# Kernel tuning notes

Hardware: AMD Instinct MI355X
Metric: run time of the kernel (lower is better)

Reference implementation:

```python
import jax, jax.numpy as jnp
import numpy as np

D_MODEL = 1024
NUM_HEADS = 16
D_K = D_MODEL // NUM_HEADS
SCALE = 1.0 / (D_K ** 0.5)


def setup_inputs() -> dict:
    key = jax.random.key(0)
    k1, k2, k3 = jax.random.split(key, 3)
    x = jax.random.normal(k1, (2, 2048, D_MODEL), dtype=jnp.float32)
    # torch nn.Linear weight layout: [out_features, in_features]; y = x @ W.T
    w_qkv = jax.random.normal(k2, (3 * D_MODEL, D_MODEL), dtype=jnp.float32) * (1.0 / np.sqrt(D_MODEL))
    w_out = jax.random.normal(k3, (D_MODEL, D_MODEL), dtype=jnp.float32) * (1.0 / np.sqrt(D_MODEL))
    return {"x": x, "w_qkv": w_qkv, "w_out": w_out}


def reference(x, w_qkv, w_out):
    b, s, _ = x.shape
    qkv = jnp.einsum("bsd,ed->bse", x, w_qkv)            # [b, s, 3*d_model]
    q, k, v = jnp.split(qkv, 3, axis=-1)
    # [b, s, h, d_k] -> [b, h, s, d_k]
    q = q.reshape(b, s, NUM_HEADS, D_K).transpose(0, 2, 1, 3)
    k = k.reshape(b, s, NUM_HEADS, D_K).transpose(0, 2, 1, 3)
    v = v.reshape(b, s, NUM_HEADS, D_K).transpose(0, 2, 1, 3)
    scores = jnp.einsum("bhqd,bhkd->bhqk", q, k) * SCALE   # [b, h, s, s]
    attn = jax.nn.softmax(scores, axis=-1)
    ctx = jnp.einsum("bhqk,bhkd->bhqd", attn, v)           # [b, h, s, d_k]
    ctx = ctx.transpose(0, 2, 1, 3).reshape(b, s, D_MODEL)
    return jnp.einsum("bsd,ed->bse", ctx, w_out)
```

## Files before the change

kernel.cpp:

```cpp
#include <hip/hip_runtime.h>

typedef __attribute__((ext_vector_type(8))) short bf16x8;
typedef __attribute__((ext_vector_type(4))) float f32x4;
typedef __attribute__((ext_vector_type(16))) float f32x16;
typedef __attribute__((ext_vector_type(4))) unsigned int u32x4;

#define MFMA16(A, B, C) __builtin_amdgcn_mfma_f32_16x16x32_bf16((A), (B), (C), 0, 0, 0)
#define MFMA32(A, B, C) __builtin_amdgcn_mfma_f32_32x32x16_bf16((A), (B), (C), 0, 0, 0)

static __device__ __forceinline__ unsigned short f32_to_bf16(float f) {
    unsigned int u = __builtin_bit_cast(unsigned int, f);
    u += 0x7fffu + ((u >> 16) & 1u);
    return (unsigned short)(u >> 16);
}

static __device__ __forceinline__ unsigned int cvtpk(float lo, float hi) {
    unsigned int r;
    asm("v_cvt_pk_bf16_f32 %0, %1, %2" : "=v"(r) : "v"(lo), "v"(hi));
    return r;
}

static __device__ __forceinline__ void gload16(const unsigned short* g, unsigned short* l) {
    __builtin_amdgcn_global_load_lds(
        (const __attribute__((address_space(1))) unsigned int*)g,
        (__attribute__((address_space(3))) unsigned int*)l, 16, 0, 0);
}

#define QSCALE 0.18033688011112042f

__global__ void cast3_f32_bf16(const float* __restrict__ x, const float* __restrict__ wq,
                               const float* __restrict__ wo,
                               unsigned short* __restrict__ xb, unsigned short* __restrict__ wqb,
                               unsigned short* __restrict__ wob) {
    int i = blockIdx.x * 256 + threadIdx.x;
    const float* src;
    unsigned short* dst;
    int off;
    if (i < 1048576)      { src = x;  dst = xb;  off = i; }
    else if (i < 1835008) { src = wq; dst = wqb; off = i - 1048576; }
    else                  { src = wo; dst = wob; off = i - 1835008; }
    float4 v = reinterpret_cast<const float4*>(src)[off];
    ushort4 o;
    o.x = f32_to_bf16(v.x);
    o.y = f32_to_bf16(v.y);
    o.z = f32_to_bf16(v.z);
    o.w = f32_to_bf16(v.w);
    reinterpret_cast<ushort4*>(dst)[off] = o;
}

template <int MODE>
__global__ __launch_bounds__(256, 2)
void gemm_bt(const unsigned short* __restrict__ Ag,
             const unsigned short* __restrict__ Bg,
             int N, int K,
             unsigned short* __restrict__ qO,
             unsigned short* __restrict__ kO,
             unsigned short* __restrict__ vO,
             float* __restrict__ fO)
{
    constexpr int BM = 128, BN = 128, BK = 64;
    __shared__ unsigned short sA[BM * BK];
    __shared__ unsigned short sB[BN * BK];

    const int m0 = blockIdx.y * BM;
    const int n0 = blockIdx.x * BN;
    const int t = threadIdx.x;
    const int lane = t & 63;
    const int wid = t >> 6;
    const int wr = wid >> 1, wc = wid & 1;
    const int g = lane >> 4, r = lane & 15;
    const int lr8 = lane >> 3, lc = lane & 7;

    const f32x4 fzero = {0.f, 0.f, 0.f, 0.f};
    f32x4 acc[4][4];
#pragma unroll
    for (int mi = 0; mi < 4; ++mi)
#pragma unroll
        for (int ni = 0; ni < 4; ++ni) acc[mi][ni] = fzero;

    for (int k0 = 0; k0 < K; k0 += BK) {
        __syncthreads();
#pragma unroll
        for (int rep = 0; rep < 4; ++rep) {
            const int rbase = rep * 32 + wid * 8;
            const int row = rbase + lr8;
            const int cs = lc ^ (row & 7);
            gload16(&Ag[(size_t)(m0 + row) * K + k0 + cs * 8], &sA[rbase * 64]);
            gload16(&Bg[(size_t)(n0 + row) * K + k0 + cs * 8], &sB[rbase * 64]);
        }
        __syncthreads();

#pragma unroll
        for (int ks = 0; ks < BK; ks += 32) {
            const int c = (ks >> 3) + g;
            bf16x8 af[4], bfr[4];
#pragma unroll
            for (int mi = 0; mi < 4; ++mi) {
                const int row = wr * 64 + mi * 16 + r;
                af[mi] = *reinterpret_cast<const bf16x8*>(&sA[row * BK + ((c * 8) ^ ((row & 7) * 8))]);
            }
#pragma unroll
            for (int ni = 0; ni < 4; ++ni) {
                const int row = wc * 64 + ni * 16 + r;
                bfr[ni] = *reinterpret_cast<const bf16x8*>(&sB[row * BK + ((c * 8) ^ ((row & 7) * 8))]);
            }
#pragma unroll
            for (int mi = 0; mi < 4; ++mi)
#pragma unroll
                for (int ni = 0; ni < 4; ++ni)
                    acc[mi][ni] = MFMA16(af[mi], bfr[ni], acc[mi][ni]);
        }
    }

#pragma unroll
    for (int mi = 0; mi < 4; ++mi) {
#pragma unroll
        for (int ni = 0; ni < 4; ++ni) {
            const int mbase = m0 + wr * 64 + mi * 16 + 4 * g;
            const int n = n0 + wc * 64 + ni * 16 + r;
            if (MODE == 0) {
                const int b = mbase >> 11, s = mbase & 2047;
                const int which = n >> 10;
                const int h = (n >> 6) & 15;
                const int d = n & 63;
                if (which == 2) {
                    ushort4 v4;
                    v4.x = f32_to_bf16(acc[mi][ni][0]);
                    v4.y = f32_to_bf16(acc[mi][ni][1]);
                    v4.z = f32_to_bf16(acc[mi][ni][2]);
                    v4.w = f32_to_bf16(acc[mi][ni][3]);
                    *reinterpret_cast<ushort4*>(&vO[(((size_t)(b * 16 + h)) * 64 + d) * 2048 + s]) = v4;
                } else {
                    const size_t dst = (((size_t)(b * 16 + h)) * 2048 + s) * 64 + d;
#pragma unroll
                    for (int i = 0; i < 4; ++i) {
                        const float val = acc[mi][ni][i];
                        if (which == 0) qO[dst + (size_t)i * 64] = f32_to_bf16(val * QSCALE);
                        else            kO[dst + (size_t)i * 64] = f32_to_bf16(val);
                    }
                }
            } else {
#pragma unroll
                for (int i = 0; i < 4; ++i)
                    fO[(size_t)(mbase + i) * N + n] = acc[mi][ni][i];
            }
        }
    }
}

__global__ __launch_bounds__(256, 2)
void attn_kernel(const unsigned short* __restrict__ Q,
                 const unsigned short* __restrict__ Kg,
                 const unsigned short* __restrict__ Vtg,
                 unsigned short* __restrict__ ctx)
{
    const int S = 2048;
    const int bid = blockIdx.x;
    const int swz = (bid & 7) * 64 + (bid >> 3);
    const int hb = swz >> 4;
    const int qb = swz & 15;
    const unsigned short* Qh = Q + (size_t)hb * S * 64;
    const unsigned short* Kh = Kg + (size_t)hb * S * 64;
    const unsigned short* Vh = Vtg + (size_t)hb * 64 * S;

    const int t = threadIdx.x, lane = t & 63, wid = t >> 6;
    const int l31 = lane & 31, lhi = lane >> 5;
    const int lr8 = lane >> 3, lc = lane & 7;
    const int q0 = qb * 128 + wid * 32;

    const int krow = (l31 & 19) | ((l31 & 4) << 1) | ((l31 & 8) >> 1);
    const int ksw = (krow & 7) ^ ((krow >> 3) & 3);
    const int vsw = (l31 & 7) ^ ((l31 >> 3) & 3);

    __shared__ unsigned short sK[2][64 * 64];
    __shared__ unsigned short sVt[2][64 * 64];

    bf16x8 qf[4];
#pragma unroll
    for (int dstep = 0; dstep < 4; ++dstep)
        qf[dstep] = *reinterpret_cast<const bf16x8*>(
            &Qh[(size_t)(q0 + l31) * 64 + dstep * 16 + lhi * 8]);

    f32x16 acc[2];
#pragma unroll
    for (int dt = 0; dt < 2; ++dt)
#pragma unroll
        for (int i = 0; i < 16; ++i) acc[dt][i] = 0.f;
    float mrun = -1e30f, lrun = 0.f;

#define STAGE(buf, k0)                                                                   \
    {                                                                                    \
        _Pragma("unroll")                                                                \
        for (int rep = 0; rep < 2; ++rep) {                                              \
            const int rbase = wid * 16 + rep * 8;                                        \
            const int row = rbase + lr8;                                                 \
            const int cs = lc ^ ((row & 7) ^ ((row >> 3) & 3));                          \
            gload16(&Kh[(size_t)((k0) + row) * 64 + cs * 8], &sK[buf][rbase * 64]);      \
            gload16(&Vh[(size_t)row * S + (k0) + cs * 8], &sVt[buf][rbase * 64]);        \
        }                                                                                \
    }

    STAGE(0, 0);
    int cur = 0;

    for (int it = 0; it < 32; ++it) {
        __syncthreads();
        if (it < 31) {
            const int kn = (it + 1) * 64;
            if (cur) STAGE(0, kn) else STAGE(1, kn);
        }

        f32x16 st0, st1;
#pragma unroll
        for (int i = 0; i < 16; ++i) { st0[i] = 0.f; st1[i] = 0.f; }
        __builtin_amdgcn_s_setprio(1);
#pragma unroll
        for (int dstep = 0; dstep < 4; ++dstep) {
            const int c = dstep * 2 + lhi;
            bf16x8 kf0 = *reinterpret_cast<const bf16x8*>(
                &sK[cur][krow * 64 + ((c ^ ksw) * 8)]);
            bf16x8 kf1 = *reinterpret_cast<const bf16x8*>(
                &sK[cur][(32 + krow) * 64 + ((c ^ ksw) * 8)]);
            st0 = MFMA32(kf0, qf[dstep], st0);
            st1 = MFMA32(kf1, qf[dstep], st1);
        }
        __builtin_amdgcn_s_setprio(0);

        float m8[8];
#pragma unroll
        for (int j = 0; j < 8; ++j)
            m8[j] = fmaxf(fmaxf(st0[j], st0[j + 8]), fmaxf(st1[j], st1[j + 8]));
        float m4a = fmaxf(m8[0], m8[1]), m4b = fmaxf(m8[2], m8[3]);
        float m4c = fmaxf(m8[4], m8[5]), m4d = fmaxf(m8[6], m8[7]);
        float mx = fmaxf(fmaxf(m4a, m4b), fmaxf(m4c, m4d));
        mx = fmaxf(mx, __shfl_xor(mx, 32));

        if (!__all(mx - mrun <= 8.f)) {
            const float mnew = fmaxf(mrun, mx);
            const float alpha = __builtin_amdgcn_exp2f(mrun - mnew);
            mrun = mnew;
            lrun *= alpha;
#pragma unroll
            for (int dt = 0; dt < 2; ++dt)
#pragma unroll
                for (int i = 0; i < 16; ++i) acc[dt][i] *= alpha;
        }

#pragma unroll
        for (int i = 0; i < 16; ++i) {
            st0[i] = __builtin_amdgcn_exp2f(st0[i] - mrun);
            st1[i] = __builtin_amdgcn_exp2f(st1[i] - mrun);
        }
        float s8[8];
#pragma unroll
        for (int j = 0; j < 8; ++j)
            s8[j] = (st0[j] + st0[j + 8]) + (st1[j] + st1[j + 8]);
        float sum = ((s8[0] + s8[1]) + (s8[2] + s8[3])) + ((s8[4] + s8[5]) + (s8[6] + s8[7]));
        sum += __shfl_xor(sum, 32);
        lrun += sum;

        bf16x8 pf[4];
#define PACK8(stv, base, out)                                                  \
        {                                                                      \
            u32x4 wv;                                                          \
            wv[0] = cvtpk(stv[(base) + 0], stv[(base) + 1]);                   \
            wv[1] = cvtpk(stv[(base) + 2], stv[(base) + 3]);                   \
            wv[2] = cvtpk(stv[(base) + 4], stv[(base) + 5]);                   \
            wv[3] = cvtpk(stv[(base) + 6], stv[(base) + 7]);                   \
            out = __builtin_bit_cast(bf16x8, wv);                              \
        }
        PACK8(st0, 0, pf[0])
        PACK8(st0, 8, pf[1])
        PACK8(st1, 0, pf[2])
        PACK8(st1, 8, pf[3])
#undef PACK8

        __builtin_amdgcn_s_setprio(1);
#pragma unroll
        for (int dt = 0; dt < 2; ++dt) {
            const int rowd = dt * 32 + l31;
#pragma unroll
            for (int ks = 0; ks < 4; ++ks) {
                const int c = ks * 2 + lhi;
                bf16x8 vf = *reinterpret_cast<const bf16x8*>(
                    &sVt[cur][rowd * 64 + ((c ^ vsw) * 8)]);
                acc[dt] = MFMA32(vf, pf[ks], acc[dt]);
            }
        }
        __builtin_amdgcn_s_setprio(0);
        cur ^= 1;
    }

    const float rl = __builtin_amdgcn_rcpf(lrun);
    const int b = hb >> 4, hh = hb & 15;
    const size_t rowbase = ((size_t)(b * 2048 + q0 + l31)) * 1024 + hh * 64;
#pragma unroll
    for (int dt = 0; dt < 2; ++dt) {
#pragma unroll
        for (int rg = 0; rg < 4; ++rg) {
            uint2 o;
            o.x = cvtpk(acc[dt][4 * rg + 0] * rl, acc[dt][4 * rg + 1] * rl);
            o.y = cvtpk(acc[dt][4 * rg + 2] * rl, acc[dt][4 * rg + 3] * rl);
            const int dbase = dt * 32 + rg * 8 + lhi * 4;
            *reinterpret_cast<uint2*>(&ctx[rowbase + dbase]) = o;
        }
    }
#undef STAGE
}

extern "C" void kernel_launch(void* const* d_in, const int* in_sizes, int n_in,
                              void* d_out, int out_size, void* d_ws, size_t ws_size,
                              hipStream_t stream) {
    const float* x     = (const float*)d_in[0];
    const float* w_qkv = (const float*)d_in[1];
    const float* w_out = (const float*)d_in[2];
    float* out = (float*)d_out;

    unsigned short* xb    = (unsigned short*)d_ws;
    unsigned short* wqkvb = xb + 4194304;
    unsigned short* woutb = wqkvb + 3145728;
    unsigned short* qB    = woutb + 1048576;
    unsigned short* kB    = qB + 4194304;
    unsigned short* vB    = kB + 4194304;
    unsigned short* ctxB  = vB + 4194304;

    cast3_f32_bf16<<<8192, 256, 0, stream>>>(x, w_qkv, w_out, xb, wqkvb, woutb);

    gemm_bt<0><<<dim3(24, 32), 256, 0, stream>>>(xb, wqkvb, 3072, 1024, qB, kB, vB, nullptr);

    attn_kernel<<<512, 256, 0, stream>>>(qB, kB, vB, ctxB);

    gemm_bt<1><<<dim3(8, 32), 256, 0, stream>>>(ctxB, woutb, 1024, 1024, nullptr, nullptr, nullptr, out);
}
```

Before: 118.7 us.

## Double-buffer GEMM LDS tiles and use smaller tiles for output projection

Templates the bf16 GEMM on tile shape and warp layout, and double-buffers the shared-memory A/B tiles so the next K-tile's global-to-LDS loads are issued before the current tile's MFMAs. The output-projection GEMM switches to 64x128 tiles with a 1x4 warp layout, doubling its grid to 512 blocks for better CU coverage. Shared memory per block doubles for the QKV GEMM (64KB), which may limit occupancy to fewer blocks per CU. Only one barrier per K-step remains, relying on the double buffer for correctness.

```diff
diff --git a/kernel.cpp b/kernel.cpp
--- a/kernel.cpp
+++ b/kernel.cpp
@@ -48,7 +48,7 @@
     reinterpret_cast<ushort4*>(dst)[off] = o;
 }
 
-template <int MODE>
+template <int MODE, int BM, int BN, int WR, int WC>
 __global__ __launch_bounds__(256, 2)
 void gemm_bt(const unsigned short* __restrict__ Ag,
              const unsigned short* __restrict__ Bg,
@@ -58,66 +58,82 @@
              unsigned short* __restrict__ vO,
              float* __restrict__ fO)
 {
-    constexpr int BM = 128, BN = 128, BK = 64;
-    __shared__ unsigned short sA[BM * BK];
-    __shared__ unsigned short sB[BN * BK];
+    constexpr int BK = 64;
+    constexpr int MFR = BM / WR / 16;
+    constexpr int NFR = BN / WC / 16;
+    __shared__ unsigned short sA[2][BM * BK];
+    __shared__ unsigned short sB[2][BN * BK];
 
     const int m0 = blockIdx.y * BM;
     const int n0 = blockIdx.x * BN;
     const int t = threadIdx.x;
     const int lane = t & 63;
     const int wid = t >> 6;
-    const int wr = wid >> 1, wc = wid & 1;
+    const int wr = wid / WC, wc = wid % WC;
     const int g = lane >> 4, r = lane & 15;
     const int lr8 = lane >> 3, lc = lane & 7;
 
     const f32x4 fzero = {0.f, 0.f, 0.f, 0.f};
-    f32x4 acc[4][4];
-#pragma unroll
-    for (int mi = 0; mi < 4; ++mi)
-#pragma unroll
-        for (int ni = 0; ni < 4; ++ni) acc[mi][ni] = fzero;
-
-    for (int k0 = 0; k0 < K; k0 += BK) {
-        __syncthreads();
-#pragma unroll
-        for (int rep = 0; rep < 4; ++rep) {
+    f32x4 acc[MFR][NFR];
+#pragma unroll
+    for (int mi = 0; mi < MFR; ++mi)
+#pragma unroll
+        for (int ni = 0; ni < NFR; ++ni) acc[mi][ni] = fzero;
+
+    auto STAGE = [&](int buf, int k0) {
+#pragma unroll
+        for (int rep = 0; rep < BM / 32; ++rep) {
             const int rbase = rep * 32 + wid * 8;
             const int row = rbase + lr8;
             const int cs = lc ^ (row & 7);
-            gload16(&Ag[(size_t)(m0 + row) * K + k0 + cs * 8], &sA[rbase * 64]);
-            gload16(&Bg[(size_t)(n0 + row) * K + k0 + cs * 8], &sB[rbase * 64]);
-        }
+            gload16(&Ag[(size_t)(m0 + row) * K + k0 + cs * 8], &sA[buf][rbase * 64]);
+        }
+#pragma unroll
+        for (int rep = 0; rep < BN / 32; ++rep) {
+            const int rbase = rep * 32 + wid * 8;
+            const int row = rbase + lr8;
+            const int cs = lc ^ (row & 7);
+            gload16(&Bg[(size_t)(n0 + row) * K + k0 + cs * 8], &sB[buf][rbase * 64]);
+        }
+    };
+
+    const int NT = K / BK;
+    STAGE(0, 0);
+    int cur = 0;
+
+    for (int kt = 0; kt < NT; ++kt) {
         __syncthreads();
+        if (kt + 1 < NT) STAGE(cur ^ 1, (kt + 1) * BK);
 
 #pragma unroll
         for (int ks = 0; ks < BK; ks += 32) {
             const int c = (ks >> 3) + g;
-            bf16x8 af[4], bfr[4];
-#pragma unroll
-            for (int mi = 0; mi < 4; ++mi) {
-                const int row = wr * 64 + mi * 16 + r;
-                af[mi] = *reinterpret_cast<const bf16x8*>(&sA[row * BK + ((c * 8) ^ ((row & 7) * 8))]);
+            bf16x8 af[MFR], bfr[NFR];
+#pragma unroll
+            for (int mi = 0; mi < MFR; ++mi) {
+                const int row = wr * (BM / WR) + mi * 16 + r;
+                af[mi] = *reinterpret_cast<const bf16x8*>(&sA[cur][row * BK + ((c * 8) ^ ((row & 7) * 8))]);
             }
 #pragma unroll
-            for (int ni = 0; ni < 4; ++ni) {
-                const int row = wc * 64 + ni * 16 + r;
-                bfr[ni] = *reinterpret_cast<const bf16x8*>(&sB[row * BK + ((c * 8) ^ ((row & 7) * 8))]);
+            for (int ni = 0; ni < NFR; ++ni) {
+                const int row = wc * (BN / WC) + ni * 16 + r;
+                bfr[ni] = *reinterpret_cast<const bf16x8*>(&sB[cur][row * BK + ((c * 8) ^ ((row & 7) * 8))]);
             }
 #pragma unroll
-            for (int mi = 0; mi < 4; ++mi)
-#pragma unroll
-                for (int ni = 0; ni < 4; ++ni)
+            for (int mi = 0; mi < MFR; ++mi)
+#pragma unroll
+                for (int ni = 0; ni < NFR; ++ni)
                     acc[mi][ni] = MFMA16(af[mi], bfr[ni], acc[mi][ni]);
         }
-    }
-
-#pragma unroll
-    for (int mi = 0; mi < 4; ++mi) {
-#pragma unroll
-        for (int ni = 0; ni < 4; ++ni) {
-            const int mbase = m0 + wr * 64 + mi * 16 + 4 * g;
-            const int n = n0 + wc * 64 + ni * 16 + r;
+        cur ^= 1;
+    }
+
+#pragma unroll
+    for (int mi = 0; mi < MFR; ++mi) {
+#pragma unroll
+        for (int ni = 0; ni < NFR; ++ni) {
+            const int mbase = m0 + wr * (BM / WR) + mi * 16 + 4 * g;
+            const int n = n0 + wc * (BN / WC) + ni * 16 + r;
             if (MODE == 0) {
                 const int b = mbase >> 11, s = mbase & 2047;
                 const int which = n >> 10;
@@ -326,9 +342,9 @@
 
     cast3_f32_bf16<<<8192, 256, 0, stream>>>(x, w_qkv, w_out, xb, wqkvb, woutb);
 
-    gemm_bt<0><<<dim3(24, 32), 256, 0, stream>>>(xb, wqkvb, 3072, 1024, qB, kB, vB, nullptr);
+    gemm_bt<0, 128, 128, 2, 2><<<dim3(24, 32), 256, 0, stream>>>(xb, wqkvb, 3072, 1024, qB, kB, vB, nullptr);
 
     attn_kernel<<<512, 256, 0, stream>>>(qB, kB, vB, ctxB);
 
-    gemm_bt<1><<<dim3(8, 32), 256, 0, stream>>>(ctxB, woutb, 1024, 1024, nullptr, nullptr, nullptr, out);
-}
+    gemm_bt<1, 64, 128, 1, 4><<<dim3(8, 64), 256, 0, stream>>>(ctxB, woutb, 1024, 1024, nullptr, nullptr, nullptr, out);
+}
```

Result: no change. 119.8 us (+1.0%).

## Split attention KV range across two wave groups with LDS softmax merge

Applied to the files above, without the earlier changes.

Each attention block now runs 8 waves instead of 4. Two halves process disjoint halves of the key/value sequence, each with its own double-buffered LDS tiles. At the end, the second half writes its partial accumulators and running max/sum to LDS, and the first half merges them with rescaling before writing ctx. This doubles wave-level parallelism per block and halves the serial loop length to hide latency, at the cost of doubled LDS use, an extra merge pass, and register pressure from the 512/4 launch bounds.

```diff
diff --git a/kernel.cpp b/kernel.cpp
--- a/kernel.cpp
+++ b/kernel.cpp
@@ -148,7 +148,7 @@
     }
 }
 
-__global__ __launch_bounds__(256, 2)
+__global__ __launch_bounds__(512, 4)
 void attn_kernel(const unsigned short* __restrict__ Q,
                  const unsigned short* __restrict__ Kg,
                  const unsigned short* __restrict__ Vtg,
@@ -164,16 +164,17 @@
     const unsigned short* Vh = Vtg + (size_t)hb * 64 * S;
 
     const int t = threadIdx.x, lane = t & 63, wid = t >> 6;
+    const int half = wid >> 2, wq = wid & 3;
     const int l31 = lane & 31, lhi = lane >> 5;
     const int lr8 = lane >> 3, lc = lane & 7;
-    const int q0 = qb * 128 + wid * 32;
+    const int q0 = qb * 128 + wq * 32;
+    const int kbase = half * 1024;
 
     const int krow = (l31 & 19) | ((l31 & 4) << 1) | ((l31 & 8) >> 1);
     const int ksw = (krow & 7) ^ ((krow >> 3) & 3);
     const int vsw = (l31 & 7) ^ ((l31 >> 3) & 3);
 
-    __shared__ unsigned short sK[2][64 * 64];
-    __shared__ unsigned short sVt[2][64 * 64];
+    __shared__ unsigned short smem[2][2][2][64 * 64];
 
     bf16x8 qf[4];
 #pragma unroll
@@ -188,27 +189,29 @@
         for (int i = 0; i < 16; ++i) acc[dt][i] = 0.f;
     float mrun = -1e30f, lrun = 0.f;
 
-#define STAGE(buf, k0)                                                                   \
-    {                                                                                    \
-        _Pragma("unroll")                                                                \
-        for (int rep = 0; rep < 2; ++rep) {                                              \
-            const int rbase = wid * 16 + rep * 8;                                        \
-            const int row = rbase + lr8;                                                 \
-            const int cs = lc ^ ((row & 7) ^ ((row >> 3) & 3));                          \
-            gload16(&Kh[(size_t)((k0) + row) * 64 + cs * 8], &sK[buf][rbase * 64]);      \
-            gload16(&Vh[(size_t)row * S + (k0) + cs * 8], &sVt[buf][rbase * 64]);        \
-        }                                                                                \
-    }
-
-    STAGE(0, 0);
-    int cur = 0;
-
-    for (int it = 0; it < 32; ++it) {
+#define STAGE(buf, k0)                                                                       \
+    {                                                                                        \
+        _Pragma("unroll")                                                                    \
+        for (int rep = 0; rep < 2; ++rep) {                                                  \
+            const int rbase = wq * 16 + rep * 8;                                             \
+            const int row = rbase + lr8;                                                     \
+            const int cs = lc ^ ((row & 7) ^ ((row >> 3) & 3));                              \
+            gload16(&Kh[(size_t)((k0) + row) * 64 + cs * 8], &smem[half][buf][0][rbase * 64]); \
+            gload16(&Vh[(size_t)row * S + (k0) + cs * 8], &smem[half][buf][1][rbase * 64]);  \
+        }                                                                                    \
+    }
+
+    STAGE(0, kbase);
+
+    for (int it = 0; it < 16; ++it) {
         __syncthreads();
-        if (it < 31) {
-            const int kn = (it + 1) * 64;
+        const int cur = it & 1;
+        if (it < 15) {
+            const int kn = kbase + (it + 1) * 64;
             if (cur) STAGE(0, kn) else STAGE(1, kn);
         }
+        const unsigned short* kb = smem[half][cur][0];
+        const unsigned short* vb = smem[half][cur][1];
 
         f32x16 st0, st1;
 #pragma unroll
@@ -217,10 +220,8 @@
 #pragma unroll
         for (int dstep = 0; dstep < 4; ++dstep) {
             const int c = dstep * 2 + lhi;
-            bf16x8 kf0 = *reinterpret_cast<const bf16x8*>(
-                &sK[cur][krow * 64 + ((c ^ ksw) * 8)]);
-            bf16x8 kf1 = *reinterpret_cast<const bf16x8*>(
-                &sK[cur][(32 + krow) * 64 + ((c ^ ksw) * 8)]);
+            bf16x8 kf0 = *reinterpret_cast<const bf16x8*>(&kb[krow * 64 + ((c ^ ksw) * 8)]);
+            bf16x8 kf1 = *reinterpret_cast<const bf16x8*>(&kb[(32 + krow) * 64 + ((c ^ ksw) * 8)]);
             st0 = MFMA32(kf0, qf[dstep], st0);
             st1 = MFMA32(kf1, qf[dstep], st1);
         }
@@ -282,30 +283,55 @@
 #pragma unroll
             for (int ks = 0; ks < 4; ++ks) {
                 const int c = ks * 2 + lhi;
-                bf16x8 vf = *reinterpret_cast<const bf16x8*>(
-                    &sVt[cur][rowd * 64 + ((c ^ vsw) * 8)]);
+                bf16x8 vf = *reinterpret_cast<const bf16x8*>(&vb[rowd * 64 + ((c ^ vsw) * 8)]);
                 acc[dt] = MFMA32(vf, pf[ks], acc[dt]);
             }
         }
         __builtin_amdgcn_s_setprio(0);
-        cur ^= 1;
-    }
-
-    const float rl = __builtin_amdgcn_rcpf(lrun);
-    const int b = hb >> 4, hh = hb & 15;
-    const size_t rowbase = ((size_t)(b * 2048 + q0 + l31)) * 1024 + hh * 64;
-#pragma unroll
-    for (int dt = 0; dt < 2; ++dt) {
-#pragma unroll
-        for (int rg = 0; rg < 4; ++rg) {
-            uint2 o;
-            o.x = cvtpk(acc[dt][4 * rg + 0] * rl, acc[dt][4 * rg + 1] * rl);
-            o.y = cvtpk(acc[dt][4 * rg + 2] * rl, acc[dt][4 * rg + 3] * rl);
-            const int dbase = dt * 32 + rg * 8 + lhi * 4;
-            *reinterpret_cast<uint2*>(&ctx[rowbase + dbase]) = o;
-        }
     }
 #undef STAGE
+
+    __syncthreads();
+    float* cb = reinterpret_cast<float*>(&smem[0][0][0][0]);
+    if (half == 1) {
+        float* base = cb + wq * 2112;
+#pragma unroll
+        for (int dt = 0; dt < 2; ++dt)
+#pragma unroll
+            for (int i = 0; i < 16; ++i)
+                base[(dt * 16 + i) * 64 + lane] = acc[dt][i];
+        if (lhi == 0) {
+            base[2048 + l31] = mrun;
+            base[2048 + 32 + l31] = lrun;
+        }
+    }
+    __syncthreads();
+    if (half == 0) {
+        float* base = cb + wq * 2112;
+        const float m1 = base[2048 + l31];
+        const float l1 = base[2048 + 32 + l31];
+        const float m = fmaxf(mrun, m1);
+        const float wA = __builtin_amdgcn_exp2f(mrun - m);
+        const float wB = __builtin_amdgcn_exp2f(m1 - m);
+        const float rl = __builtin_amdgcn_rcpf(lrun * wA + l1 * wB);
+        const int b = hb >> 4, hh = hb & 15;
+        const size_t rowbase = ((size_t)(b * 2048 + q0 + l31)) * 1024 + hh * 64;
+#pragma unroll
+        for (int dt = 0; dt < 2; ++dt) {
+#pragma unroll
+            for (int rg = 0; rg < 4; ++rg) {
+                float v0 = (acc[dt][4 * rg + 0] * wA + base[(dt * 16 + 4 * rg + 0) * 64 + lane] * wB) * rl;
+                float v1 = (acc[dt][4 * rg + 1] * wA + base[(dt * 16 + 4 * rg + 1) * 64 + lane] * wB) * rl;
+                float v2 = (acc[dt][4 * rg + 2] * wA + base[(dt * 16 + 4 * rg + 2) * 64 + lane] * wB) * rl;
+                float v3 = (acc[dt][4 * rg + 3] * wA + base[(dt * 16 + 4 * rg + 3) * 64 + lane] * wB) * rl;
+                uint2 o;
+                o.x = cvtpk(v0, v1);
+                o.y = cvtpk(v2, v3);
+                const int dbase = dt * 32 + rg * 8 + lhi * 4;
+                *reinterpret_cast<uint2*>(&ctx[rowbase + dbase]) = o;
+            }
+        }
+    }
 }
 
 extern "C" void kernel_launch(void* const* d_in, const int* in_sizes, int n_in,
@@ -328,7 +354,7 @@
 
     gemm_bt<0><<<dim3(24, 32), 256, 0, stream>>>(xb, wqkvb, 3072, 1024, qB, kB, vB, nullptr);
 
-    attn_kernel<<<512, 256, 0, stream>>>(qB, kB, vB, ctxB);
+    attn_kernel<<<512, 512, 0, stream>>>(qB, kB, vB, ctxB);
 
     gemm_bt<1><<<dim3(8, 32), 256, 0, stream>>>(ctxB, woutb, 1024, 1024, nullptr, nullptr, nullptr, out);
 }
```

After: 113.8 us. 1.04x faster.
